# Kernel optimization log

Measured on AMD Instinct MI355X. Metric: run time of the kernel, lower is better.

## Reference

```python
import jax, jax.numpy as jnp
import numpy as np

KQ = 512
NEG = -1e9


def setup_inputs() -> dict:
    key = jax.random.key(0)
    k1, k2, k3, k4, k5 = jax.random.split(key, 5)
    B, NQ, NK, D, V, O = 16, 1024, 2048, 512, 512, 256
    return {
        "keys": jax.random.normal(k1, (B, NK, D), dtype=jnp.float32),
        "queries": jax.random.normal(k2, (B, NQ, D), dtype=jnp.float32),
        "values": jax.random.normal(k3, (B, NK, V), dtype=jnp.float32),
        "mask": jax.random.randint(k4, (B, NQ, NK), 0, 2, dtype=jnp.int32),
        "W_resize": jax.random.normal(k5, (O, V), dtype=jnp.float32) * (1.0 / np.sqrt(V)),
        "b_resize": jnp.zeros((O,), dtype=jnp.float32),
    }


def reference(keys, queries, values, mask, W_resize, b_resize):
    # score: scaled dot product  [B, NQ, NK]
    logits = jnp.einsum("bqd,bkd->bqk", queries, keys) / jnp.sqrt(jnp.float32(KQ))
    logits = jnp.where(mask == 0, jnp.float32(NEG), logits)
    attn = jax.nn.softmax(logits, axis=-1)
    # context: [B, NQ, V]
    context = jnp.einsum("bqk,bkv->bqv", attn, values)
    # resize to out_size
    context = jnp.einsum("bqv,ov->bqo", context, W_resize) + b_resize
    return context
```

## Files before the change

kernel.cpp:

```cpp
#include <hip/hip_runtime.h>

#define BB   16
#define NQ   1024
#define NK   2048
#define DD   512
#define VV   512
#define OO   256
#define SCALE 0.044194173824159216f

typedef __attribute__((ext_vector_type(4))) float f32x4;
typedef __attribute__((ext_vector_type(8))) short s16x8;

#define AS1(p) ((const __attribute__((address_space(1))) void*)(p))
#define AS3(p) ((__attribute__((address_space(3))) void*)(p))

__device__ __forceinline__ unsigned short f2bf(float f) {
  unsigned u = __float_as_uint(f);
  u += 0x7fffu + ((u >> 16) & 1u);
  return (unsigned short)(u >> 16);
}
__device__ __forceinline__ float bf2f(unsigned short b) {
  return __uint_as_float(((unsigned)b) << 16);
}

#define MFMA16(a, b, c) __builtin_amdgcn_mfma_f32_16x16x32_bf16(a, b, c, 0, 0, 0)

__device__ __forceinline__ void gemm_bt_core(
    const unsigned short* __restrict__ Abase,
    const unsigned short* __restrict__ Bbase,
    int K,
    unsigned short* As, unsigned short* Bs,
    f32x4 acc[4][4])
{
  const int t = threadIdx.x;
  const int w = t >> 6;
  const int l = t & 63;
  const int srow = l >> 2;
  const int scol = (l & 3) * 8;
  const int r0 = (w * 2 + 0) * 16 + srow;
  const int r1 = (w * 2 + 1) * 16 + srow;
  const int lds0 = (w * 2 + 0) * 512 + l * 8;
  const int lds1 = (w * 2 + 1) * 512 + l * 8;
  const int wm = (w >> 1) * 64;
  const int wn = (w & 1) * 64;
  const int lm = l & 15;
  const int lq = l >> 4;

  for (int kt = 0; kt < K; kt += 32) {
    __builtin_amdgcn_global_load_lds(AS1(Abase + (size_t)r0 * K + kt + scol), AS3(As + lds0), 16, 0, 0);
    __builtin_amdgcn_global_load_lds(AS1(Abase + (size_t)r1 * K + kt + scol), AS3(As + lds1), 16, 0, 0);
    __builtin_amdgcn_global_load_lds(AS1(Bbase + (size_t)r0 * K + kt + scol), AS3(Bs + lds0), 16, 0, 0);
    __builtin_amdgcn_global_load_lds(AS1(Bbase + (size_t)r1 * K + kt + scol), AS3(Bs + lds1), 16, 0, 0);
    __syncthreads();
    s16x8 af[4], bfr[4];
    #pragma unroll
    for (int i = 0; i < 4; ++i) {
      af[i]  = *(const s16x8*)(As + (wm + i * 16 + lm) * 32 + lq * 8);
      bfr[i] = *(const s16x8*)(Bs + (wn + i * 16 + lm) * 32 + lq * 8);
    }
    #pragma unroll
    for (int mi = 0; mi < 4; ++mi)
      #pragma unroll
      for (int ni = 0; ni < 4; ++ni)
        acc[mi][ni] = MFMA16(af[mi], bfr[ni], acc[mi][ni]);
    __syncthreads();
  }
}


#define CS_STRIDE 136

__global__ __launch_bounds__(256)
void qkvw_kernel(const unsigned short* __restrict__ Qb,
                 const unsigned short* __restrict__ Kb,
                 const unsigned short* __restrict__ Vb,
                 const unsigned short* __restrict__ Wb,
                 const int* __restrict__ mask,
                 unsigned short* __restrict__ P,
                 unsigned short* __restrict__ VWt,
                 float* __restrict__ sums)
{
  __shared__ unsigned short smem[128 * CS_STRIDE];
  unsigned short* As = smem;
  unsigned short* Bs = smem + 4096;
  unsigned short* Cs = smem;
  const int bid = blockIdx.x;
  const int t = threadIdx.x, w = t >> 6, l = t & 63;
  const int wm = (w >> 1) * 64, wn = (w & 1) * 64;
  const int lm = l & 15, lq = l >> 4;
  const int trow = t >> 4, tcol = (t & 15) * 8;

  f32x4 acc[4][4];
  #pragma unroll
  for (int i = 0; i < 4; ++i)
    #pragma unroll
    for (int j = 0; j < 4; ++j) acc[i][j] = (f32x4){0.f, 0.f, 0.f, 0.f};

  if (bid < 2048) {
    const int b  = bid >> 7;
    const int tm = (bid >> 4) & 7;
    const int tn = bid & 15;

    gemm_bt_core(Qb + ((size_t)b * NQ + tm * 128) * DD,
                 Kb + ((size_t)b * NK + tn * 128) * DD, DD, As, Bs, acc);

    #pragma unroll
    for (int mi = 0; mi < 4; ++mi)
      #pragma unroll
      for (int ni = 0; ni < 4; ++ni)
        #pragma unroll
        for (int r = 0; r < 4; ++r)
          Cs[(wm + mi * 16 + lq * 4 + r) * CS_STRIDE + wn + ni * 16 + lm] =
              f2bf(acc[mi][ni][r] * SCALE);
    __syncthreads();

    #pragma unroll
    for (int it = 0; it < 8; ++it) {
      const int row = it * 16 + trow;
      const int gq = tm * 128 + row;
      const size_t gbase = ((size_t)b * NQ + gq) * NK + tn * 128 + tcol;
      s16x8 v = *(const s16x8*)(Cs + row * CS_STRIDE + tcol);
      const int4 m0 = *(const int4*)(mask + gbase);
      const int4 m1 = *(const int4*)(mask + gbase + 4);
      float e[8];
      e[0] = m0.x ? __expf(bf2f((unsigned short)v[0])) : 0.f;
      e[1] = m0.y ? __expf(bf2f((unsigned short)v[1])) : 0.f;
      e[2] = m0.z ? __expf(bf2f((unsigned short)v[2])) : 0.f;
      e[3] = m0.w ? __expf(bf2f((unsigned short)v[3])) : 0.f;
      e[4] = m1.x ? __expf(bf2f((unsigned short)v[4])) : 0.f;
      e[5] = m1.y ? __expf(bf2f((unsigned short)v[5])) : 0.f;
      e[6] = m1.z ? __expf(bf2f((unsigned short)v[6])) : 0.f;
      e[7] = m1.w ? __expf(bf2f((unsigned short)v[7])) : 0.f;
      float sp = 0.f;
      #pragma unroll
      for (int j = 0; j < 8; ++j) sp += e[j];
      #pragma unroll
      for (int off = 8; off > 0; off >>= 1) sp += __shfl_down(sp, off, 16);
      if ((t & 15) == 0) atomicAdd(&sums[(size_t)b * NQ + gq], sp);
      s16x8 o;
      #pragma unroll
      for (int j = 0; j < 8; ++j) o[j] = (short)f2bf(e[j]);
      *(s16x8*)(P + gbase) = o;
    }
  } else {
    const int vid = bid - 2048;
    const int b  = vid >> 5;
    const int kt = (vid >> 1) & 15;
    const int ot = vid & 1;

    gemm_bt_core(Vb + ((size_t)b * NK + kt * 128) * VV,
                 Wb + (size_t)ot * 128 * VV, VV, As, Bs, acc);

    #pragma unroll
    for (int mi = 0; mi < 4; ++mi)
      #pragma unroll
      for (int ni = 0; ni < 4; ++ni)
        #pragma unroll
        for (int r = 0; r < 4; ++r)
          Cs[(wn + ni * 16 + lm) * CS_STRIDE + wm + mi * 16 + lq * 4 + r] =
              f2bf(acc[mi][ni][r]);
    __syncthreads();

    #pragma unroll
    for (int it = 0; it < 8; ++it) {
      const int orow = it * 16 + trow;
      s16x8 v = *(const s16x8*)(Cs + orow * CS_STRIDE + tcol);
      *(s16x8*)(VWt + ((size_t)b * OO + ot * 128 + orow) * NK + kt * 128 + tcol) = v;
    }
  }
}

#define PW_STRIDE 132
__global__ __launch_bounds__(256)
void pvw_kernel(const unsigned short* __restrict__ P,
                const unsigned short* __restrict__ VWt,
                const float* __restrict__ sums,
                const float* __restrict__ bias,
                float* __restrict__ out)
{
  const int ot = blockIdx.x;
  const int qt = blockIdx.y;
  const int b  = blockIdx.z;
  __shared__ float Csf[64 * PW_STRIDE];
  __shared__ float Ls[64];
  unsigned short* As = (unsigned short*)Csf;
  unsigned short* Bs = (unsigned short*)Csf + 2048;

  const int t = threadIdx.x, w = t >> 6, l = t & 63;
  const int wr = w >> 1, wc = w & 1;
  const int lm = l & 15, lq = l >> 4;
  if (t < 64) Ls[t] = 1.0f / sums[(size_t)b * NQ + qt * 64 + t];

  f32x4 acc[2][4];
  #pragma unroll
  for (int i = 0; i < 2; ++i)
    #pragma unroll
    for (int j = 0; j < 4; ++j) acc[i][j] = (f32x4){0.f, 0.f, 0.f, 0.f};

  const unsigned short* Abase = P   + ((size_t)b * NQ + qt * 64) * NK;
  const unsigned short* Bbase = VWt + ((size_t)b * OO + ot * 128) * NK;
  const int ar = t >> 2, ac = (t & 3) * 8;
  const int br0 = (w * 2 + 0) * 16 + (l >> 2);
  const int br1 = (w * 2 + 1) * 16 + (l >> 2);
  const int bc = (l & 3) * 8;
  const int bld0 = (w * 2 + 0) * 512 + l * 8;
  const int bld1 = (w * 2 + 1) * 512 + l * 8;

  for (int k0 = 0; k0 < NK; k0 += 32) {
    __builtin_amdgcn_global_load_lds(AS1(Abase + (size_t)ar * NK + k0 + ac), AS3(As + t * 8), 16, 0, 0);
    __builtin_amdgcn_global_load_lds(AS1(Bbase + (size_t)br0 * NK + k0 + bc), AS3(Bs + bld0), 16, 0, 0);
    __builtin_amdgcn_global_load_lds(AS1(Bbase + (size_t)br1 * NK + k0 + bc), AS3(Bs + bld1), 16, 0, 0);
    __syncthreads();
    s16x8 af[2], bfr[4];
    #pragma unroll
    for (int mi = 0; mi < 2; ++mi)
      af[mi] = *(const s16x8*)(As + (wr * 32 + mi * 16 + lm) * 32 + lq * 8);
    #pragma unroll
    for (int ni = 0; ni < 4; ++ni)
      bfr[ni] = *(const s16x8*)(Bs + (wc * 64 + ni * 16 + lm) * 32 + lq * 8);
    #pragma unroll
    for (int mi = 0; mi < 2; ++mi)
      #pragma unroll
      for (int ni = 0; ni < 4; ++ni)
        acc[mi][ni] = MFMA16(af[mi], bfr[ni], acc[mi][ni]);
    __syncthreads();
  }

  #pragma unroll
  for (int mi = 0; mi < 2; ++mi)
    #pragma unroll
    for (int ni = 0; ni < 4; ++ni)
      #pragma unroll
      for (int r = 0; r < 4; ++r) {
        const int row = wr * 32 + mi * 16 + lq * 4 + r;
        const int col = wc * 64 + ni * 16 + lm;
        Csf[row * PW_STRIDE + col] = acc[mi][ni][r] * Ls[row];
      }
  __syncthreads();
  const int trow = t >> 2;
  #pragma unroll
  for (int it = 0; it < 4; ++it) {
    const int col = (t & 3) * 8 + it * 32;
    f32x4 a = *(const f32x4*)(Csf + trow * PW_STRIDE + col);
    f32x4 c = *(const f32x4*)(Csf + trow * PW_STRIDE + col + 4);
    const int go = ot * 128 + col;
    a += *(const f32x4*)(bias + go);
    c += *(const f32x4*)(bias + go + 4);
    float* o = out + ((size_t)b * NQ + qt * 64 + trow) * OO + go;
    *(f32x4*)o = a;
    *(f32x4*)(o + 4) = c;
  }
}

__device__ __forceinline__ void cvt8(const float* __restrict__ in,
                                     unsigned short* __restrict__ out, int i)
{
  const float4* p = (const float4*)in + (size_t)i * 2;
  const float4 a = p[0], b = p[1];
  s16x8 o;
  o[0] = (short)f2bf(a.x); o[1] = (short)f2bf(a.y);
  o[2] = (short)f2bf(a.z); o[3] = (short)f2bf(a.w);
  o[4] = (short)f2bf(b.x); o[5] = (short)f2bf(b.y);
  o[6] = (short)f2bf(b.z); o[7] = (short)f2bf(b.w);
  ((s16x8*)out)[i] = o;
}

__global__ __launch_bounds__(256)
void prep_kernel(const float* __restrict__ q, const float* __restrict__ k,
                 const float* __restrict__ v, const float* __restrict__ w,
                 unsigned short* __restrict__ Qb, unsigned short* __restrict__ Kb,
                 unsigned short* __restrict__ Vb, unsigned short* __restrict__ Wb,
                 float* __restrict__ sums)
{
  const int bid = blockIdx.x;
  const int t = threadIdx.x;
  if (bid < 4096) {
    cvt8(q, Qb, bid * 256 + t);
  } else if (bid < 12288) {
    cvt8(k, Kb, (bid - 4096) * 256 + t);
  } else if (bid < 20480) {
    cvt8(v, Vb, (bid - 12288) * 256 + t);
  } else if (bid < 20544) {
    cvt8(w, Wb, (bid - 20480) * 256 + t);
  } else {
    const int i = (bid - 20544) * 256 + t;
    if (i < BB * NQ) sums[i] = 0.f;
  }
}

extern "C" void kernel_launch(void* const* d_in, const int* in_sizes, int n_in,
                              void* d_out, int out_size, void* d_ws, size_t ws_size,
                              hipStream_t stream)
{
  const float* keys    = (const float*)d_in[0];
  const float* queries = (const float*)d_in[1];
  const float* values  = (const float*)d_in[2];
  const int*   mask    = (const int*)  d_in[3];
  const float* W       = (const float*)d_in[4];
  const float* bias    = (const float*)d_in[5];
  float* out = (float*)d_out;

  char* ws = (char*)d_ws;
  unsigned short* Qb  = (unsigned short*)(ws);
  unsigned short* Kb  = (unsigned short*)(ws + (16ull << 20));
  unsigned short* Vb  = (unsigned short*)(ws + (48ull << 20));
  unsigned short* Wb  = (unsigned short*)(ws + (80ull << 20));
  unsigned short* VWt = (unsigned short*)(ws + (81ull << 20));
  unsigned short* P   = (unsigned short*)(ws + (97ull << 20));
  float* sums         = (float*)(ws + (161ull << 20));

  prep_kernel<<<dim3(20608), 256, 0, stream>>>(queries, keys, values, W,
                                               Qb, Kb, Vb, Wb, sums);
  qkvw_kernel<<<dim3(2560), 256, 0, stream>>>(Qb, Kb, Vb, Wb, mask, P, VWt, sums);
  pvw_kernel<<<dim3(OO / 128, NQ / 64, BB), 256, 0, stream>>>(P, VWt, sums, bias, out);
}
```

Baseline: 427.6 us.

## Double-buffer LDS tiles in both GEMMs and swizzle wider PV tiles

Both GEMM main loops now use two LDS buffers. The next K-tile's global_load_lds is issued before the MFMAs on the current tile, so each iteration needs only one barrier instead of two, and load latency can overlap compute. The PV kernel also doubles its K-step to 64 and applies an XOR swizzle to the LDS layout, meant to cut bank conflicts on fragment reads. The trade-off is more shared memory per block (about 48KB in the PV kernel), which may lower occupancy.

```diff
diff --git a/kernel.cpp b/kernel.cpp
--- a/kernel.cpp
+++ b/kernel.cpp
@@ -29,7 +29,7 @@
     const unsigned short* __restrict__ Abase,
     const unsigned short* __restrict__ Bbase,
     int K,
-    unsigned short* As, unsigned short* Bs,
+    unsigned short* smem,
     f32x4 acc[4][4])
 {
   const int t = threadIdx.x;
@@ -39,19 +39,29 @@
   const int scol = (l & 3) * 8;
   const int r0 = (w * 2 + 0) * 16 + srow;
   const int r1 = (w * 2 + 1) * 16 + srow;
-  const int lds0 = (w * 2 + 0) * 512 + l * 8;
-  const int lds1 = (w * 2 + 1) * 512 + l * 8;
+  const int ld0 = (w * 2 + 0) * 512 + l * 8;
+  const int ld1 = (w * 2 + 1) * 512 + l * 8;
   const int wm = (w >> 1) * 64;
   const int wn = (w & 1) * 64;
   const int lm = l & 15;
   const int lq = l >> 4;
 
+#define QK_STAGE(buf, kt) do {                                                             \
+    unsigned short* As_ = smem + (buf) * 8192;                                             \
+    unsigned short* Bs_ = As_ + 4096;                                                      \
+    __builtin_amdgcn_global_load_lds(AS1(Abase + (size_t)r0 * K + (kt) + scol), AS3(As_ + ld0), 16, 0, 0); \
+    __builtin_amdgcn_global_load_lds(AS1(Abase + (size_t)r1 * K + (kt) + scol), AS3(As_ + ld1), 16, 0, 0); \
+    __builtin_amdgcn_global_load_lds(AS1(Bbase + (size_t)r0 * K + (kt) + scol), AS3(Bs_ + ld0), 16, 0, 0); \
+    __builtin_amdgcn_global_load_lds(AS1(Bbase + (size_t)r1 * K + (kt) + scol), AS3(Bs_ + ld1), 16, 0, 0); \
+  } while (0)
+
+  QK_STAGE(0, 0);
+  __syncthreads();
   for (int kt = 0; kt < K; kt += 32) {
-    __builtin_amdgcn_global_load_lds(AS1(Abase + (size_t)r0 * K + kt + scol), AS3(As + lds0), 16, 0, 0);
-    __builtin_amdgcn_global_load_lds(AS1(Abase + (size_t)r1 * K + kt + scol), AS3(As + lds1), 16, 0, 0);
-    __builtin_amdgcn_global_load_lds(AS1(Bbase + (size_t)r0 * K + kt + scol), AS3(Bs + lds0), 16, 0, 0);
-    __builtin_amdgcn_global_load_lds(AS1(Bbase + (size_t)r1 * K + kt + scol), AS3(Bs + lds1), 16, 0, 0);
-    __syncthreads();
+    const int cur = (kt >> 5) & 1;
+    if (kt + 32 < K) QK_STAGE(cur ^ 1, kt + 32);
+    const unsigned short* As = smem + cur * 8192;
+    const unsigned short* Bs = As + 4096;
     s16x8 af[4], bfr[4];
     #pragma unroll
     for (int i = 0; i < 4; ++i) {
@@ -65,6 +75,7 @@
         acc[mi][ni] = MFMA16(af[mi], bfr[ni], acc[mi][ni]);
     __syncthreads();
   }
+#undef QK_STAGE
 }
 
 
@@ -80,9 +91,7 @@
                  unsigned short* __restrict__ VWt,
                  float* __restrict__ sums)
 {
-  __shared__ unsigned short smem[128 * CS_STRIDE];
-  unsigned short* As = smem;
-  unsigned short* Bs = smem + 4096;
+  __shared__ unsigned short smem[17408];
   unsigned short* Cs = smem;
   const int bid = blockIdx.x;
   const int t = threadIdx.x, w = t >> 6, l = t & 63;
@@ -102,7 +111,7 @@
     const int tn = bid & 15;
 
     gemm_bt_core(Qb + ((size_t)b * NQ + tm * 128) * DD,
-                 Kb + ((size_t)b * NK + tn * 128) * DD, DD, As, Bs, acc);
+                 Kb + ((size_t)b * NK + tn * 128) * DD, DD, smem, acc);
 
     #pragma unroll
     for (int mi = 0; mi < 4; ++mi)
@@ -149,7 +158,7 @@
     const int ot = vid & 1;
 
     gemm_bt_core(Vb + ((size_t)b * NK + kt * 128) * VV,
-                 Wb + (size_t)ot * 128 * VV, VV, As, Bs, acc);
+                 Wb + (size_t)ot * 128 * VV, VV, smem, acc);
 
     #pragma unroll
     for (int mi = 0; mi < 4; ++mi)
@@ -181,10 +190,8 @@
   const int ot = blockIdx.x;
   const int qt = blockIdx.y;
   const int b  = blockIdx.z;
-  __shared__ float Csf[64 * PW_STRIDE];
+  __shared__ unsigned short smem[24576];
   __shared__ float Ls[64];
-  unsigned short* As = (unsigned short*)Csf;
-  unsigned short* Bs = (unsigned short*)Csf + 2048;
 
   const int t = threadIdx.x, w = t >> 6, l = t & 63;
   const int wr = w >> 1, wc = w & 1;
@@ -199,33 +206,56 @@
 
   const unsigned short* Abase = P   + ((size_t)b * NQ + qt * 64) * NK;
   const unsigned short* Bbase = VWt + ((size_t)b * OO + ot * 128) * NK;
-  const int ar = t >> 2, ac = (t & 3) * 8;
-  const int br0 = (w * 2 + 0) * 16 + (l >> 2);
-  const int br1 = (w * 2 + 1) * 16 + (l >> 2);
-  const int bc = (l & 3) * 8;
-  const int bld0 = (w * 2 + 0) * 512 + l * 8;
-  const int bld1 = (w * 2 + 1) * 512 + l * 8;
-
-  for (int k0 = 0; k0 < NK; k0 += 32) {
-    __builtin_amdgcn_global_load_lds(AS1(Abase + (size_t)ar * NK + k0 + ac), AS3(As + t * 8), 16, 0, 0);
-    __builtin_amdgcn_global_load_lds(AS1(Bbase + (size_t)br0 * NK + k0 + bc), AS3(Bs + bld0), 16, 0, 0);
-    __builtin_amdgcn_global_load_lds(AS1(Bbase + (size_t)br1 * NK + k0 + bc), AS3(Bs + bld1), 16, 0, 0);
+
+  const int srow = t >> 3;
+  const int ssc  = (((t & 7) ^ (srow & 7)) << 3);
+
+#define PV_STAGE(buf, k0v) do {                                                            \
+    unsigned short* As_ = smem + (buf) * 12288;                                            \
+    unsigned short* Bs_ = As_ + 4096;                                                      \
+    const int k0_ = (k0v);                                                                 \
+    __builtin_amdgcn_global_load_lds(AS1(Abase + (size_t)(srow     ) * NK + k0_ + ssc), AS3(As_ +        t * 8), 16, 0, 0); \
+    __builtin_amdgcn_global_load_lds(AS1(Abase + (size_t)(srow + 32) * NK + k0_ + ssc), AS3(As_ + 2048 + t * 8), 16, 0, 0); \
+    __builtin_amdgcn_global_load_lds(AS1(Bbase + (size_t)(srow     ) * NK + k0_ + ssc), AS3(Bs_ +        t * 8), 16, 0, 0); \
+    __builtin_amdgcn_global_load_lds(AS1(Bbase + (size_t)(srow + 32) * NK + k0_ + ssc), AS3(Bs_ + 2048 + t * 8), 16, 0, 0); \
+    __builtin_amdgcn_global_load_lds(AS1(Bbase + (size_t)(srow + 64) * NK + k0_ + ssc), AS3(Bs_ + 4096 + t * 8), 16, 0, 0); \
+    __builtin_amdgcn_global_load_lds(AS1(Bbase + (size_t)(srow + 96) * NK + k0_ + ssc), AS3(Bs_ + 6144 + t * 8), 16, 0, 0); \
+  } while (0)
+
+  PV_STAGE(0, 0);
+  __syncthreads();
+  for (int k0 = 0; k0 < NK; k0 += 64) {
+    const int cur = (k0 >> 6) & 1;
+    if (k0 + 64 < NK) PV_STAGE(cur ^ 1, k0 + 64);
+    const unsigned short* As = smem + cur * 12288;
+    const unsigned short* Bs = As + 4096;
+    s16x8 af[2][2], bfr[4][2];
+    #pragma unroll
+    for (int mi = 0; mi < 2; ++mi) {
+      const int row = wr * 32 + mi * 16 + lm;
+      #pragma unroll
+      for (int ks = 0; ks < 2; ++ks)
+        af[mi][ks] = *(const s16x8*)(As + row * 64 + (((ks * 4 + lq) ^ (row & 7)) << 3));
+    }
+    #pragma unroll
+    for (int ni = 0; ni < 4; ++ni) {
+      const int row = wc * 64 + ni * 16 + lm;
+      #pragma unroll
+      for (int ks = 0; ks < 2; ++ks)
+        bfr[ni][ks] = *(const s16x8*)(Bs + row * 64 + (((ks * 4 + lq) ^ (row & 7)) << 3));
+    }
+    #pragma unroll
+    for (int mi = 0; mi < 2; ++mi)
+      #pragma unroll
+      for (int ni = 0; ni < 4; ++ni) {
+        acc[mi][ni] = MFMA16(af[mi][0], bfr[ni][0], acc[mi][ni]);
+        acc[mi][ni] = MFMA16(af[mi][1], bfr[ni][1], acc[mi][ni]);
+      }
     __syncthreads();
-    s16x8 af[2], bfr[4];
-    #pragma unroll
-    for (int mi = 0; mi < 2; ++mi)
-      af[mi] = *(const s16x8*)(As + (wr * 32 + mi * 16 + lm) * 32 + lq * 8);
-    #pragma unroll
-    for (int ni = 0; ni < 4; ++ni)
-      bfr[ni] = *(const s16x8*)(Bs + (wc * 64 + ni * 16 + lm) * 32 + lq * 8);
-    #pragma unroll
-    for (int mi = 0; mi < 2; ++mi)
-      #pragma unroll
-      for (int ni = 0; ni < 4; ++ni)
-        acc[mi][ni] = MFMA16(af[mi], bfr[ni], acc[mi][ni]);
-    __syncthreads();
-  }
-
+  }
+#undef PV_STAGE
+
+  float* Csf = (float*)smem;
   #pragma unroll
   for (int mi = 0; mi < 2; ++mi)
     #pragma unroll
```

New measurement: 417.2 us. -2.4%, faster.
